# Performance work log

Hardware: AMD Instinct MI355X
Metric: run time of the kernel (lower is better)

The kernel has to match this reference:

```python
import jax, jax.numpy as jnp
import numpy as np
import math

V, D, H, L, T, B = 32000, 768, 12, 4, 1024, 2
HD = D // H  # head size 64
EMB_SCALE = math.sqrt(D)  # DynamicTanh path
EPS = 1e-5


def setup_inputs() -> dict:
    key = jax.random.key(0)
    ks = jax.random.split(key, 10)
    def rn(k, shape, std=0.02):
        return jax.random.normal(k, shape, jnp.float32) * std
    return {
        "idx": jax.random.randint(ks[0], (B, T), 0, V, dtype=jnp.int32).astype(jnp.int64) if False else jax.random.randint(ks[0], (B, T), 0, V),
        "wte": rn(ks[1], (V, D)),            # tied with lm_head
        "wpe": rn(ks[2], (T, D)),            # block_size == T
        "ln1_alpha": jnp.full((L, 1), 0.5, jnp.float32),
        "ln1_w": jnp.ones((L, D), jnp.float32),
        "ln1_b": jnp.zeros((L, D), jnp.float32),
        "wq": rn(ks[3], (L, D, D)),          # stored [in,out] (torch W.T)
        "wk": rn(ks[4], (L, D, D)),
        "wv": rn(ks[5], (L, D, D)),
        "wo": rn(ks[6], (L, D, D)),
        "bo": jnp.zeros((L, D), jnp.float32),
        "ln2_alpha": jnp.full((L, 1), 0.5, jnp.float32),
        "ln2_w": jnp.ones((L, D), jnp.float32),
        "ln2_b": jnp.zeros((L, D), jnp.float32),
        "w_fc": rn(ks[7], (L, D, 4 * D)),
        "b_fc": jnp.zeros((L, 4 * D), jnp.float32),
        "w_proj": rn(ks[8], (L, 4 * D, D), std=0.02 / math.sqrt(2 * L)),
        "b_proj": jnp.zeros((L, D), jnp.float32),
        "lnf_alpha": jnp.full((1,), 0.5, jnp.float32),
        "lnf_w": jnp.ones((D,), jnp.float32),
        "lnf_b": jnp.zeros((D,), jnp.float32),
    }


def _dyt(x, alpha, w, b):
    # DynamicTanh: layernorm-style normalize, then w * tanh(alpha * xn) + b
    mu = x.mean(-1, keepdims=True)
    var = ((x - mu) ** 2).mean(-1, keepdims=True)
    xn = (x - mu) * jax.lax.rsqrt(var + EPS)
    return w * jnp.tanh(alpha * xn) + b


def reference(idx, wte, wpe, ln1_alpha, ln1_w, ln1_b, wq, wk, wv, wo, bo,
              ln2_alpha, ln2_w, ln2_b, w_fc, b_fc, w_proj, b_proj,
              lnf_alpha, lnf_w, lnf_b):
    Bb, Tt = idx.shape
    x = (wte[idx] + wpe[:Tt][None]) * EMB_SCALE          # [B,T,D]; dropout = eval identity
    mask = jnp.tril(jnp.ones((Tt, Tt), bool))
    scale = 1.0 / math.sqrt(HD)
    for l in range(L):
        h = _dyt(x, ln1_alpha[l], ln1_w[l], ln1_b[l])
        q = (h @ wq[l]).reshape(Bb, Tt, H, HD)
        k = (h @ wk[l]).reshape(Bb, Tt, H, HD)
        v = (h @ wv[l]).reshape(Bb, Tt, H, HD)
        att = jnp.einsum('bqhd,bkhd->bhqk', q, k) * scale
        att = jnp.where(mask, att, -jnp.inf)
        att = jax.nn.softmax(att, axis=-1)
        o = jnp.einsum('bhqk,bkhd->bqhd', att, v).reshape(Bb, Tt, D)
        x = x + o @ wo[l] + bo[l]
        h = _dyt(x, ln2_alpha[l], ln2_w[l], ln2_b[l])
        h = jax.nn.gelu(h @ w_fc[l] + b_fc[l], approximate=False)  # torch nn.GELU = exact erf
        x = x + h @ w_proj[l] + b_proj[l]
    x = _dyt(x, lnf_alpha, lnf_w, lnf_b)
    return x @ wte.T                                     # tied lm_head, [B,T,V]
```

## Files before the change

kernel.cpp:

```cpp
#include <hip/hip_runtime.h>
#include <hip/hip_bf16.h>
#include <math.h>

constexpr int B_ = 2, T_ = 1024, D_ = 768, H_ = 12, L_ = 4, V_ = 32000;
constexpr int M_ = B_ * T_;
constexpr int FF_ = 4 * D_;
constexpr int QKVN_ = 3 * D_;
#define EMB_SCALE 27.712812921102035f
#define EPS_ 1e-5f

typedef __attribute__((ext_vector_type(8))) short short8_t;
typedef __attribute__((ext_vector_type(4))) float float4_t;

__device__ __forceinline__ float bf2f(__hip_bfloat16 v) { return __bfloat162float(v); }
__device__ __forceinline__ __hip_bfloat16 f2bf(float v) { return __float2bfloat16(v); }

__device__ __forceinline__ void gl_lds16(const __hip_bfloat16* g, __hip_bfloat16* l) {
    __builtin_amdgcn_global_load_lds(
        (const __attribute__((address_space(1))) void*)g,
        (__attribute__((address_space(3))) void*)l, 16, 0, 0);
}

__global__ __launch_bounds__(256) void convert_kernel(
    const float* __restrict__ src, __hip_bfloat16* __restrict__ dst, size_t n)
{
    size_t i = ((size_t)blockIdx.x * 256 + threadIdx.x) * 4;
    if (i + 3 < n) {
        float4 f = *(const float4*)(src + i);
        dst[i + 0] = f2bf(f.x);
        dst[i + 1] = f2bf(f.y);
        dst[i + 2] = f2bf(f.z);
        dst[i + 3] = f2bf(f.w);
    }
}

__global__ __launch_bounds__(256) void tconv_kernel(
    const float* __restrict__ src, __hip_bfloat16* __restrict__ dst,
    int K, int N, size_t sstride, size_t dstride)
{
    __shared__ float tile[32][33];
    const float* S = src + (size_t)blockIdx.z * sstride;
    __hip_bfloat16* Dd = dst + (size_t)blockIdx.z * dstride;
    int n0 = blockIdx.x * 32, k0 = blockIdx.y * 32;
    int tx = threadIdx.x & 31, ty = threadIdx.x >> 5;
#pragma unroll
    for (int i = 0; i < 32; i += 8)
        tile[ty + i][tx] = S[(size_t)(k0 + ty + i) * N + n0 + tx];
    __syncthreads();
#pragma unroll
    for (int i = 0; i < 32; i += 8)
        Dd[(size_t)(n0 + ty + i) * K + k0 + tx] = f2bf(tile[tx][ty + i]);
}

__global__ __launch_bounds__(256) void embed_kernel(
    const int* __restrict__ idx, const float* __restrict__ wte,
    const float* __restrict__ wpe, float* __restrict__ x)
{
    int row = blockIdx.x, tid = threadIdx.x;
    int t = row & (T_ - 1);
    int tok = idx[row];
#pragma unroll
    for (int i = 0; i < 3; ++i) {
        int c = i * 256 + tid;
        x[(size_t)row * D_ + c] =
            (wte[(size_t)tok * D_ + c] + wpe[(size_t)t * D_ + c]) * EMB_SCALE;
    }
}

__global__ __launch_bounds__(256) void dyt_kernel(
    const float* __restrict__ x, __hip_bfloat16* __restrict__ h,
    const float* __restrict__ w, const float* __restrict__ bb,
    const float* __restrict__ alpha_p)
{
    const int row = blockIdx.x, tid = threadIdx.x;
    const float* xr = x + (size_t)row * D_;
    float v[3];
    float s = 0.f, ss = 0.f;
#pragma unroll
    for (int i = 0; i < 3; ++i) {
        v[i] = xr[i * 256 + tid];
        s += v[i];
        ss += v[i] * v[i];
    }
#pragma unroll
    for (int off = 32; off >= 1; off >>= 1) {
        s  += __shfl_xor(s,  off, 64);
        ss += __shfl_xor(ss, off, 64);
    }
    __shared__ float sh[8];
    int wave = tid >> 6;
    if ((tid & 63) == 0) { sh[wave] = s; sh[wave + 4] = ss; }
    __syncthreads();
    s  = sh[0] + sh[1] + sh[2] + sh[3];
    ss = sh[4] + sh[5] + sh[6] + sh[7];
    float mu = s * (1.f / D_);
    float var = ss * (1.f / D_) - mu * mu;
    float rstd = rsqrtf(var + EPS_);
    float alpha = *alpha_p;
#pragma unroll
    for (int i = 0; i < 3; ++i) {
        int c = i * 256 + tid;
        float xn = (v[i] - mu) * rstd;
        h[(size_t)row * D_ + c] = f2bf(w[c] * tanhf(alpha * xn) + bb[c]);
    }
}

constexpr int LSTR = 72;

__global__ __launch_bounds__(256) void fattn_kernel(
    const __hip_bfloat16* __restrict__ qkv, __hip_bfloat16* __restrict__ o)
{
    const int qt = gridDim.x - 1 - blockIdx.x;
    const int hh = blockIdx.y, b = blockIdx.z;
    const int q0 = qt * 64;
    const int tid = threadIdx.x;
    const int wave = tid >> 6, lane = tid & 63;
    const int quad = lane >> 4, l16 = lane & 15;
    const size_t rs = QKVN_;

    __shared__ __hip_bfloat16 Ks[64 * LSTR];
    __shared__ __hip_bfloat16 Vts[64 * LSTR];
    __shared__ __hip_bfloat16 Ps[4][16 * LSTR];

    const __hip_bfloat16* qrow = qkv + (size_t)(b * T_ + q0 + wave * 16 + l16) * rs + hh * 64;
    short8_t qf0 = *(const short8_t*)(qrow + quad * 8);
    short8_t qf1 = *(const short8_t*)(qrow + 32 + quad * 8);

    float4_t Oacc[4];
#pragma unroll
    for (int j = 0; j < 4; ++j) Oacc[j] = (float4_t){0.f, 0.f, 0.f, 0.f};
    float mrow[4], lrow[4];
#pragma unroll
    for (int r = 0; r < 4; ++r) { mrow[r] = -1e30f; lrow[r] = 0.f; }

    const __hip_bfloat16* kbase = qkv + (size_t)b * T_ * rs + D_ + hh * 64;
    const __hip_bfloat16* vbase = qkv + (size_t)b * T_ * rs + 2 * D_ + hh * 64;

    const int sr = tid >> 2;
    const int sc = (tid & 3) * 8;
    const int vr = lane;
    const int vc0 = wave * 16;

    for (int kt = 0; kt <= qt; ++kt) {
        const int kt0 = kt * 64;
        uint4 kv0 = *(const uint4*)(kbase + (size_t)(kt0 + sr) * rs + sc);
        uint4 kv1 = *(const uint4*)(kbase + (size_t)(kt0 + sr) * rs + sc + 32);
        uint4 vv0 = *(const uint4*)(vbase + (size_t)(kt0 + vr) * rs + vc0);
        uint4 vv1 = *(const uint4*)(vbase + (size_t)(kt0 + vr) * rs + vc0 + 8);
        __syncthreads();
        *(uint4*)(Ks + sr * LSTR + sc)      = kv0;
        *(uint4*)(Ks + sr * LSTR + sc + 32) = kv1;
        {
            const __hip_bfloat16* vp = (const __hip_bfloat16*)&vv0;
#pragma unroll
            for (int i = 0; i < 8; ++i) Vts[(vc0 + i) * LSTR + vr] = vp[i];
            vp = (const __hip_bfloat16*)&vv1;
#pragma unroll
            for (int i = 0; i < 8; ++i) Vts[(vc0 + 8 + i) * LSTR + vr] = vp[i];
        }
        __syncthreads();

        float4_t S[4];
#pragma unroll
        for (int jt = 0; jt < 4; ++jt) {
            short8_t kf0 = *(const short8_t*)(Ks + (jt * 16 + l16) * LSTR + quad * 8);
            short8_t kf1 = *(const short8_t*)(Ks + (jt * 16 + l16) * LSTR + 32 + quad * 8);
            float4_t s = (float4_t){0.f, 0.f, 0.f, 0.f};
            s = __builtin_amdgcn_mfma_f32_16x16x32_bf16(qf0, kf0, s, 0, 0, 0);
            s = __builtin_amdgcn_mfma_f32_16x16x32_bf16(qf1, kf1, s, 0, 0, 0);
            S[jt] = s;
        }

        if (kt == qt) {
#pragma unroll
            for (int jt = 0; jt < 4; ++jt)
#pragma unroll
                for (int r = 0; r < 4; ++r) {
                    int qg = wave * 16 + quad * 4 + r;
                    int kg = jt * 16 + l16;
                    S[jt][r] = (kg > qg) ? -1e30f : S[jt][r] * 0.125f;
                }
        } else {
#pragma unroll
            for (int jt = 0; jt < 4; ++jt)
#pragma unroll
                for (int r = 0; r < 4; ++r) S[jt][r] *= 0.125f;
        }

        float mnew[4], alphav[4];
#pragma unroll
        for (int r = 0; r < 4; ++r) {
            float mx = fmaxf(fmaxf(S[0][r], S[1][r]), fmaxf(S[2][r], S[3][r]));
            mx = fmaxf(mx, __shfl_xor(mx, 1, 64));
            mx = fmaxf(mx, __shfl_xor(mx, 2, 64));
            mx = fmaxf(mx, __shfl_xor(mx, 4, 64));
            mx = fmaxf(mx, __shfl_xor(mx, 8, 64));
            mnew[r] = fmaxf(mrow[r], mx);
            alphav[r] = __expf(mrow[r] - mnew[r]);
            mrow[r] = mnew[r];
        }
        float psum[4] = {0.f, 0.f, 0.f, 0.f};
#pragma unroll
        for (int jt = 0; jt < 4; ++jt)
#pragma unroll
            for (int r = 0; r < 4; ++r) {
                float p = __expf(S[jt][r] - mnew[r]);
                S[jt][r] = p;
                psum[r] += p;
            }
#pragma unroll
        for (int r = 0; r < 4; ++r) {
            float ps = psum[r];
            ps += __shfl_xor(ps, 1, 64);
            ps += __shfl_xor(ps, 2, 64);
            ps += __shfl_xor(ps, 4, 64);
            ps += __shfl_xor(ps, 8, 64);
            lrow[r] = lrow[r] * alphav[r] + ps;
        }

        __hip_bfloat16* ps_base = Ps[wave];
#pragma unroll
        for (int jt = 0; jt < 4; ++jt)
#pragma unroll
            for (int r = 0; r < 4; ++r)
                ps_base[(quad * 4 + r) * LSTR + jt * 16 + l16] = f2bf(S[jt][r]);

#pragma unroll
        for (int j = 0; j < 4; ++j)
#pragma unroll
            for (int r = 0; r < 4; ++r) Oacc[j][r] *= alphav[r];

        short8_t pf0 = *(const short8_t*)(ps_base + l16 * LSTR + quad * 8);
        short8_t pf1 = *(const short8_t*)(ps_base + l16 * LSTR + 32 + quad * 8);
#pragma unroll
        for (int j = 0; j < 4; ++j) {
            short8_t vf0 = *(const short8_t*)(Vts + (j * 16 + l16) * LSTR + quad * 8);
            short8_t vf1 = *(const short8_t*)(Vts + (j * 16 + l16) * LSTR + 32 + quad * 8);
            Oacc[j] = __builtin_amdgcn_mfma_f32_16x16x32_bf16(pf0, vf0, Oacc[j], 0, 0, 0);
            Oacc[j] = __builtin_amdgcn_mfma_f32_16x16x32_bf16(pf1, vf1, Oacc[j], 0, 0, 0);
        }
    }

    float inv_l[4];
#pragma unroll
    for (int r = 0; r < 4; ++r) inv_l[r] = 1.f / lrow[r];
    __hip_bfloat16* orow = o + (size_t)(b * T_ + q0 + wave * 16) * D_ + hh * 64;
#pragma unroll
    for (int j = 0; j < 4; ++j)
#pragma unroll
        for (int r = 0; r < 4; ++r)
            orow[(size_t)(quad * 4 + r) * D_ + j * 16 + l16] = f2bf(Oacc[j][r] * inv_l[r]);
}

__device__ __forceinline__ float gelu_exact(float t) {
    return 0.5f * t * (1.0f + erff(t * 0.70710678118654752f));
}

template <int EPI>
__global__ __launch_bounds__(256, 2) void gemm_bt(
    const __hip_bfloat16* __restrict__ A, const __hip_bfloat16* __restrict__ Bt,
    float* __restrict__ outF, __hip_bfloat16* __restrict__ outB,
    const float* __restrict__ bias, const float* __restrict__ res,
    int M, int N, int K)
{
    __shared__ __hip_bfloat16 As[128 * 32];
    __shared__ __hip_bfloat16 Bs[128 * 32];
    const int tid = threadIdx.x;
    const int wave = tid >> 6, lane = tid & 63;
    const int quad = lane >> 4, l16 = lane & 15;
    const int m0 = blockIdx.y * 128, n0 = blockIdx.x * 128;
    const int wm = (wave >> 1) * 64, wn = (wave & 1) * 64;

    float4_t acc[4][4];
#pragma unroll
    for (int i = 0; i < 4; ++i)
#pragma unroll
        for (int j = 0; j < 4; ++j) acc[i][j] = (float4_t){0.f, 0.f, 0.f, 0.f};

    const int lr = lane >> 2, lc = (lane & 3) * 8;
    const __hip_bfloat16* ga0 = A  + (size_t)(m0 + wave * 16 + lr) * K + lc;
    const __hip_bfloat16* ga1 = A  + (size_t)(m0 + 64 + wave * 16 + lr) * K + lc;
    const __hip_bfloat16* gb0 = Bt + (size_t)(n0 + wave * 16 + lr) * K + lc;
    const __hip_bfloat16* gb1 = Bt + (size_t)(n0 + 64 + wave * 16 + lr) * K + lc;
    __hip_bfloat16* la0 = As + (wave * 16) * 32;
    __hip_bfloat16* la1 = As + (64 + wave * 16) * 32;
    __hip_bfloat16* lb0 = Bs + (wave * 16) * 32;
    __hip_bfloat16* lb1 = Bs + (64 + wave * 16) * 32;

    for (int k0 = 0; k0 < K; k0 += 32) {
        __syncthreads();
        gl_lds16(ga0 + k0, la0);
        gl_lds16(ga1 + k0, la1);
        gl_lds16(gb0 + k0, lb0);
        gl_lds16(gb1 + k0, lb1);
        __syncthreads();
        short8_t af[4], bfv[4];
#pragma unroll
        for (int i = 0; i < 4; ++i) {
            af[i]  = *(const short8_t*)(As + (wm + i * 16 + l16) * 32 + quad * 8);
            bfv[i] = *(const short8_t*)(Bs + (wn + i * 16 + l16) * 32 + quad * 8);
        }
#pragma unroll
        for (int i = 0; i < 4; ++i)
#pragma unroll
            for (int j = 0; j < 4; ++j)
                acc[i][j] = __builtin_amdgcn_mfma_f32_16x16x32_bf16(
                    af[i], bfv[j], acc[i][j], 0, 0, 0);
    }

#pragma unroll
    for (int i = 0; i < 4; ++i) {
#pragma unroll
        for (int j = 0; j < 4; ++j) {
            int colg = n0 + wn + j * 16 + l16;
#pragma unroll
            for (int rg = 0; rg < 4; ++rg) {
                int rowg = m0 + wm + i * 16 + quad * 4 + rg;
                size_t offo = (size_t)rowg * N + colg;
                float v = acc[i][j][rg];
                if (EPI == 0) {
                    outB[offo] = f2bf(v);
                } else if (EPI == 1) {
                    outF[offo] = res[offo] + v + bias[colg];
                } else if (EPI == 2) {
                    outB[offo] = f2bf(gelu_exact(v + bias[colg]));
                } else {
                    outF[offo] = v;
                }
            }
        }
    }
}

__global__ __launch_bounds__(512, 2) void gemm_lmhead(
    const __hip_bfloat16* __restrict__ A, const __hip_bfloat16* __restrict__ Bt,
    float* __restrict__ out)
{
    constexpr int K = D_;
    constexpr int N = V_;
    constexpr int NT = K / 32;
    __shared__ __hip_bfloat16 lds[32768];

    const int tid  = threadIdx.x;
    const int wave = tid >> 6, lane = tid & 63;
    const int quad = lane >> 4, l16 = lane & 15;

    const int flat = blockIdx.x;
    const int g = (flat & 7) * 125 + (flat >> 3);
    const int m0 = (g & 7) * 256, n0 = (g >> 3) * 256;

    const int wm = (wave >> 2) * 128;
    const int wn = (wave & 3) * 64;

    const int slr  = tid >> 2;
    const int sq   = (tid & 3) ^ ((slr >> 1) & 3);
    const int rbase = ((slr & 64) << 1) | (slr & 63);
    const __hip_bfloat16* gA = A  + (size_t)(m0 + rbase) * K + sq * 8;
    const __hip_bfloat16* gB = Bt + (size_t)(n0 + rbase) * K + sq * 8;
    const int wb = wave * 1024;
    char* ldsc = (char*)lds;

#define STG(gp, Xoff, hh, tt) \
    gl_lds16((gp) + (size_t)(hh) * 64 * K + (tt) * 32, \
             (__hip_bfloat16*)(ldsc + (((tt) & 1) * 32768 + (Xoff) + (hh) * 8192 + wb)))

    const int xe   = (quad ^ ((l16 >> 1) & 3)) * 16;
    const int aoff = wm * 32 + l16 * 64 + xe;
    const int boff = 16384 + ((wn >> 6) & 1) * 8192 + (wn & 128) * 32 + l16 * 64 + xe;

    float4_t acc[8][4];
#pragma unroll
    for (int i = 0; i < 8; ++i)
#pragma unroll
        for (int j = 0; j < 4; ++j) acc[i][j] = (float4_t){0.f, 0.f, 0.f, 0.f};

    STG(gA, 0,     0, 0); STG(gB, 16384, 0, 0);
    STG(gA, 0,     1, 0); STG(gB, 16384, 1, 0);
    STG(gA, 0,     0, 1); STG(gB, 16384, 0, 1);
    asm volatile("s_waitcnt vmcnt(2)" ::: "memory");
    __builtin_amdgcn_sched_barrier(0);
    __builtin_amdgcn_s_barrier();

    auto do_tile = [&](int tt, bool last2) {
        const char* base = ldsc + (tt & 1) * 32768;
        short8_t af[4], bf[4];
#pragma unroll
        for (int ii = 0; ii < 4; ++ii)
            af[ii] = *(const short8_t*)(base + ii * 1024 + aoff);
#pragma unroll
        for (int j = 0; j < 4; ++j)
            bf[j] = *(const short8_t*)(base + j * 1024 + boff);
        if (tt + 1 < NT) { STG(gA, 0, 1, tt + 1); STG(gB, 16384, 1, tt + 1); }
        __builtin_amdgcn_s_barrier();
        asm volatile("s_waitcnt lgkmcnt(0)" ::: "memory");
        __builtin_amdgcn_sched_barrier(0);
        __builtin_amdgcn_s_setprio(1);
#pragma unroll
        for (int ii = 0; ii < 4; ++ii)
#pragma unroll
            for (int j = 0; j < 4; ++j)
                acc[ii][j] = __builtin_amdgcn_mfma_f32_16x16x32_bf16(
                    af[ii], bf[j], acc[ii][j], 0, 0, 0);
        __builtin_amdgcn_s_setprio(0);
        __builtin_amdgcn_s_barrier();
#pragma unroll
        for (int ii = 0; ii < 4; ++ii)
            af[ii] = *(const short8_t*)(base + 8192 + ii * 1024 + aoff);
        if (tt + 2 < NT) { STG(gA, 0, 0, tt + 2); STG(gB, 16384, 0, tt + 2); }
        __builtin_amdgcn_s_barrier();
        asm volatile("s_waitcnt lgkmcnt(0)" ::: "memory");
        __builtin_amdgcn_sched_barrier(0);
        __builtin_amdgcn_s_setprio(1);
#pragma unroll
        for (int ii = 0; ii < 4; ++ii)
#pragma unroll
            for (int j = 0; j < 4; ++j)
                acc[4 + ii][j] = __builtin_amdgcn_mfma_f32_16x16x32_bf16(
                    af[ii], bf[j], acc[4 + ii][j], 0, 0, 0);
        __builtin_amdgcn_s_setprio(0);
        if (last2) {
            asm volatile("s_waitcnt vmcnt(0)" ::: "memory");
        } else {
            asm volatile("s_waitcnt vmcnt(2)" ::: "memory");
        }
        __builtin_amdgcn_sched_barrier(0);
        __builtin_amdgcn_s_barrier();
    };

    for (int t = 0; t + 2 < NT; t += 2) { do_tile(t, false); do_tile(t + 1, false); }
    do_tile(NT - 2, true);
    do_tile(NT - 1, false);
#undef STG

    float* orow = out + (size_t)(m0 + wm + quad * 4) * N + (n0 + wn + l16);
#pragma unroll
    for (int i = 0; i < 8; ++i)
#pragma unroll
        for (int j = 0; j < 4; ++j)
#pragma unroll
            for (int rg = 0; rg < 4; ++rg)
                orow[(size_t)(i * 16 + rg) * N + j * 16] = acc[i][j][rg];
}

extern "C" void kernel_launch(void* const* d_in, const int* in_sizes, int n_in,
                              void* d_out, int out_size, void* d_ws, size_t ws_size,
                              hipStream_t stream)
{
    const int*   idx   = (const int*)d_in[0];
    const float* wte   = (const float*)d_in[1];
    const float* wpe   = (const float*)d_in[2];
    const float* ln1_a = (const float*)d_in[3];
    const float* ln1_w = (const float*)d_in[4];
    const float* ln1_b = (const float*)d_in[5];
    const float* wq    = (const float*)d_in[6];
    const float* wk    = (const float*)d_in[7];
    const float* wv    = (const float*)d_in[8];
    const float* wo    = (const float*)d_in[9];
    const float* bo    = (const float*)d_in[10];
    const float* ln2_a = (const float*)d_in[11];
    const float* ln2_w = (const float*)d_in[12];
    const float* ln2_b = (const float*)d_in[13];
    const float* w_fc  = (const float*)d_in[14];
    const float* b_fc  = (const float*)d_in[15];
    const float* w_pr  = (const float*)d_in[16];
    const float* b_pr  = (const float*)d_in[17];
    const float* lnf_a = (const float*)d_in[18];
    const float* lnf_w = (const float*)d_in[19];
    const float* lnf_b = (const float*)d_in[20];
    float* out = (float*)d_out;

    char* ws = (char*)d_ws;
    size_t off = 0;
    auto alloc = [&](size_t bytes) -> char* {
        char* p = ws + off;
        off += (bytes + 255) & ~(size_t)255;
        return p;
    };
    __hip_bfloat16* wqkv_t = (__hip_bfloat16*)alloc((size_t)L_ * QKVN_ * D_ * 2);
    __hip_bfloat16* wo_t   = (__hip_bfloat16*)alloc((size_t)L_ * D_ * D_ * 2);
    __hip_bfloat16* wfc_t  = (__hip_bfloat16*)alloc((size_t)L_ * FF_ * D_ * 2);
    __hip_bfloat16* wpr_t  = (__hip_bfloat16*)alloc((size_t)L_ * D_ * FF_ * 2);
    __hip_bfloat16* wte_b  = (__hip_bfloat16*)alloc((size_t)V_ * D_ * 2);
    float*          x      = (float*)alloc((size_t)M_ * D_ * 4);
    __hip_bfloat16* h      = (__hip_bfloat16*)alloc((size_t)M_ * D_ * 2);
    __hip_bfloat16* qkv    = (__hip_bfloat16*)alloc((size_t)M_ * QKVN_ * 2);
    __hip_bfloat16* attno  = (__hip_bfloat16*)alloc((size_t)M_ * D_ * 2);
    __hip_bfloat16* mid    = (__hip_bfloat16*)alloc((size_t)M_ * FF_ * 2);
    (void)ws_size; (void)in_sizes; (void)n_in; (void)out_size;

    {
        size_t n = (size_t)V_ * D_;
        convert_kernel<<<dim3((unsigned)(n / 1024)), 256, 0, stream>>>(wte, wte_b, n);
    }
    size_t wstride = (size_t)D_ * D_;
    tconv_kernel<<<dim3(24, 24, L_), 256, 0, stream>>>(wq, wqkv_t + 0,            D_, D_, wstride, (size_t)QKVN_ * D_);
    tconv_kernel<<<dim3(24, 24, L_), 256, 0, stream>>>(wk, wqkv_t + (size_t)D_ * D_,   D_, D_, wstride, (size_t)QKVN_ * D_);
    tconv_kernel<<<dim3(24, 24, L_), 256, 0, stream>>>(wv, wqkv_t + (size_t)2 * D_ * D_, D_, D_, wstride, (size_t)QKVN_ * D_);
    tconv_kernel<<<dim3(24, 24, L_), 256, 0, stream>>>(wo, wo_t,                  D_, D_, wstride, wstride);
    tconv_kernel<<<dim3(96, 24, L_), 256, 0, stream>>>(w_fc, wfc_t, D_, FF_, (size_t)D_ * FF_, (size_t)FF_ * D_);
    tconv_kernel<<<dim3(24, 96, L_), 256, 0, stream>>>(w_pr, wpr_t, FF_, D_, (size_t)FF_ * D_, (size_t)D_ * FF_);

    embed_kernel<<<dim3(M_), 256, 0, stream>>>(idx, wte, wpe, x);

    for (int l = 0; l < L_; ++l) {
        dyt_kernel<<<dim3(M_), 256, 0, stream>>>(x, h, ln1_w + l * D_, ln1_b + l * D_, ln1_a + l);
        gemm_bt<0><<<dim3(QKVN_ / 128, M_ / 128), 256, 0, stream>>>(
            h, wqkv_t + (size_t)l * QKVN_ * D_, nullptr, qkv, nullptr, nullptr, M_, QKVN_, D_);
        fattn_kernel<<<dim3(T_ / 64, H_, B_), 256, 0, stream>>>(qkv, attno);
        gemm_bt<1><<<dim3(D_ / 128, M_ / 128), 256, 0, stream>>>(
            attno, wo_t + (size_t)l * D_ * D_, x, nullptr, bo + l * D_, x, M_, D_, D_);
        dyt_kernel<<<dim3(M_), 256, 0, stream>>>(x, h, ln2_w + l * D_, ln2_b + l * D_, ln2_a + l);
        gemm_bt<2><<<dim3(FF_ / 128, M_ / 128), 256, 0, stream>>>(
            h, wfc_t + (size_t)l * FF_ * D_, nullptr, mid, b_fc + l * FF_, nullptr, M_, FF_, D_);
        gemm_bt<1><<<dim3(D_ / 128, M_ / 128), 256, 0, stream>>>(
            mid, wpr_t + (size_t)l * D_ * FF_, x, nullptr, b_pr + l * D_, x, M_, D_, FF_);
    }

    dyt_kernel<<<dim3(M_), 256, 0, stream>>>(x, h, lnf_w, lnf_b, lnf_a);
    gemm_lmhead<<<dim3((M_ / 256) * (V_ / 256)), 512, 0, stream>>>(h, wte_b, out);
}
```

Before: 1.275 ms.

## Add 4-stage LDS ring prefetch with XOR swizzle to layer GEMMs

Replaces the single-buffered gemm_bt loop, which synchronised twice per K-step, with a 4-slot LDS ring. Async global-to-LDS loads run three tiles ahead and are gated by explicit vmcnt waits, leaving one barrier per iteration. It also XOR-swizzles the LDS layout to cut bank conflicts on fragment reads, and raises wave priority around the MFMA block. LDS use grows to 64KB per block, which may cap occupancy at the intended 2 blocks per CU.

```diff
diff --git a/kernel.cpp b/kernel.cpp
--- a/kernel.cpp
+++ b/kernel.cpp
@@ -257,19 +257,37 @@
 }
 
 template <int EPI>
-__global__ __launch_bounds__(256, 2) void gemm_bt(
+__global__ __launch_bounds__(256, 2) void gemm_btp(
     const __hip_bfloat16* __restrict__ A, const __hip_bfloat16* __restrict__ Bt,
     float* __restrict__ outF, __hip_bfloat16* __restrict__ outB,
     const float* __restrict__ bias, const float* __restrict__ res,
     int M, int N, int K)
 {
-    __shared__ __hip_bfloat16 As[128 * 32];
-    __shared__ __hip_bfloat16 Bs[128 * 32];
+    __shared__ __hip_bfloat16 lds[4 * 8192];
     const int tid = threadIdx.x;
     const int wave = tid >> 6, lane = tid & 63;
     const int quad = lane >> 4, l16 = lane & 15;
     const int m0 = blockIdx.y * 128, n0 = blockIdx.x * 128;
     const int wm = (wave >> 1) * 64, wn = (wave & 1) * 64;
+    const int NT = K >> 5;
+
+    const int srow = tid >> 2;
+    const int sq   = (tid & 3) ^ ((srow >> 1) & 3);
+    const __hip_bfloat16* gA = A  + (size_t)(m0 + srow) * K + sq * 8;
+    const __hip_bfloat16* gB = Bt + (size_t)(n0 + srow) * K + sq * 8;
+    char* ldsc = (char*)lds;
+    const int wb = wave * 1024;
+
+#define STGP(tt) do {                                                      \
+        const size_t ko = (size_t)(tt) * 32;                               \
+        char* bb = ldsc + ((tt) & 3) * 16384 + wb;                         \
+        gl_lds16(gA + ko,                  (__hip_bfloat16*)(bb));         \
+        gl_lds16(gA + (size_t)64 * K + ko, (__hip_bfloat16*)(bb + 4096));  \
+        gl_lds16(gB + ko,                  (__hip_bfloat16*)(bb + 8192));  \
+        gl_lds16(gB + (size_t)64 * K + ko, (__hip_bfloat16*)(bb + 12288)); \
+    } while (0)
+
+    const int xe = (quad ^ ((l16 >> 1) & 3)) * 16;
 
     float4_t acc[4][4];
 #pragma unroll
@@ -277,36 +295,42 @@
 #pragma unroll
         for (int j = 0; j < 4; ++j) acc[i][j] = (float4_t){0.f, 0.f, 0.f, 0.f};
 
-    const int lr = lane >> 2, lc = (lane & 3) * 8;
-    const __hip_bfloat16* ga0 = A  + (size_t)(m0 + wave * 16 + lr) * K + lc;
-    const __hip_bfloat16* ga1 = A  + (size_t)(m0 + 64 + wave * 16 + lr) * K + lc;
-    const __hip_bfloat16* gb0 = Bt + (size_t)(n0 + wave * 16 + lr) * K + lc;
-    const __hip_bfloat16* gb1 = Bt + (size_t)(n0 + 64 + wave * 16 + lr) * K + lc;
-    __hip_bfloat16* la0 = As + (wave * 16) * 32;
-    __hip_bfloat16* la1 = As + (64 + wave * 16) * 32;
-    __hip_bfloat16* lb0 = Bs + (wave * 16) * 32;
-    __hip_bfloat16* lb1 = Bs + (64 + wave * 16) * 32;
-
-    for (int k0 = 0; k0 < K; k0 += 32) {
-        __syncthreads();
-        gl_lds16(ga0 + k0, la0);
-        gl_lds16(ga1 + k0, la1);
-        gl_lds16(gb0 + k0, lb0);
-        gl_lds16(gb1 + k0, lb1);
-        __syncthreads();
+    STGP(0); STGP(1); STGP(2);
+    asm volatile("s_waitcnt vmcnt(8)" ::: "memory");
+    __builtin_amdgcn_sched_barrier(0);
+    __builtin_amdgcn_s_barrier();
+
+    for (int t = 0; t < NT; ++t) {
+        if (t + 3 < NT) STGP(t + 3);
+        const char* base = ldsc + (t & 3) * 16384;
         short8_t af[4], bfv[4];
 #pragma unroll
-        for (int i = 0; i < 4; ++i) {
-            af[i]  = *(const short8_t*)(As + (wm + i * 16 + l16) * 32 + quad * 8);
-            bfv[i] = *(const short8_t*)(Bs + (wn + i * 16 + l16) * 32 + quad * 8);
-        }
+        for (int i = 0; i < 4; ++i)
+            af[i]  = *(const short8_t*)(base + (wm + i * 16 + l16) * 64 + xe);
+#pragma unroll
+        for (int j = 0; j < 4; ++j)
+            bfv[j] = *(const short8_t*)(base + 8192 + (wn + j * 16 + l16) * 64 + xe);
+        asm volatile("s_waitcnt lgkmcnt(0)" ::: "memory");
+        __builtin_amdgcn_sched_barrier(0);
+        __builtin_amdgcn_s_setprio(1);
 #pragma unroll
         for (int i = 0; i < 4; ++i)
 #pragma unroll
             for (int j = 0; j < 4; ++j)
                 acc[i][j] = __builtin_amdgcn_mfma_f32_16x16x32_bf16(
                     af[i], bfv[j], acc[i][j], 0, 0, 0);
-    }
+        __builtin_amdgcn_s_setprio(0);
+        if (t + 3 < NT) {
+            asm volatile("s_waitcnt vmcnt(8)" ::: "memory");
+        } else if (t + 2 < NT) {
+            asm volatile("s_waitcnt vmcnt(4)" ::: "memory");
+        } else if (t + 1 < NT) {
+            asm volatile("s_waitcnt vmcnt(0)" ::: "memory");
+        }
+        __builtin_amdgcn_sched_barrier(0);
+        __builtin_amdgcn_s_barrier();
+    }
+#undef STGP
 
 #pragma unroll
     for (int i = 0; i < 4; ++i) {
@@ -504,15 +528,15 @@
 
     for (int l = 0; l < L_; ++l) {
         dyt_kernel<<<dim3(M_), 256, 0, stream>>>(x, h, ln1_w + l * D_, ln1_b + l * D_, ln1_a + l);
-        gemm_bt<0><<<dim3(QKVN_ / 128, M_ / 128), 256, 0, stream>>>(
+        gemm_btp<0><<<dim3(QKVN_ / 128, M_ / 128), 256, 0, stream>>>(
             h, wqkv_t + (size_t)l * QKVN_ * D_, nullptr, qkv, nullptr, nullptr, M_, QKVN_, D_);
         fattn_kernel<<<dim3(T_ / 64, H_, B_), 256, 0, stream>>>(qkv, attno);
-        gemm_bt<1><<<dim3(D_ / 128, M_ / 128), 256, 0, stream>>>(
+        gemm_btp<1><<<dim3(D_ / 128, M_ / 128), 256, 0, stream>>>(
             attno, wo_t + (size_t)l * D_ * D_, x, nullptr, bo + l * D_, x, M_, D_, D_);
         dyt_kernel<<<dim3(M_), 256, 0, stream>>>(x, h, ln2_w + l * D_, ln2_b + l * D_, ln2_a + l);
-        gemm_bt<2><<<dim3(FF_ / 128, M_ / 128), 256, 0, stream>>>(
+        gemm_btp<2><<<dim3(FF_ / 128, M_ / 128), 256, 0, stream>>>(
             h, wfc_t + (size_t)l * FF_ * D_, nullptr, mid, b_fc + l * FF_, nullptr, M_, FF_, D_);
-        gemm_bt<1><<<dim3(D_ / 128, M_ / 128), 256, 0, stream>>>(
+        gemm_btp<1><<<dim3(D_ / 128, M_ / 128), 256, 0, stream>>>(
             mid, wpr_t + (size_t)l * D_ * FF_, x, nullptr, b_pr + l * D_, x, M_, D_, FF_);
     }
 
```

Result: faster. 1.126 ms (-11.7%).
